# Performance work log

Hardware: AMD Instinct MI355X
Metric: run time of the kernel (lower is better)

Reference implementation:

```python
import jax, jax.numpy as jnp
import numpy as np

B, P, C = 2, 512, 21          # images, proposals/image, classes (incl background)
REG = 5                       # xc, yc, w, h, angle(deg)
DET = 100                     # detections_per_img
IMW, IMH = 1024, 800
SCORE_THRESH = 0.05
NMS_THR = 0.5
WEIGHTS = (10.0, 10.0, 5.0, 5.0, 3.0)
BBOX_XFORM_CLIP = float(np.log(1000.0 / 16.0))
MAXV = 8                      # max vertices of quad-quad intersection


def setup_inputs() -> dict:
    key = jax.random.key(0)
    k1, k2, k3 = jax.random.split(key, 3)
    class_logits = jax.random.normal(k1, (B * P, C), jnp.float32)
    box_regression = jax.random.normal(k2, (B * P, C * REG), jnp.float32)
    u = jax.random.uniform(k3, (B * P, 5), jnp.float32)
    rrects = jnp.stack([
        u[:, 0] * IMW,            # xc
        u[:, 1] * IMH,            # yc
        u[:, 2] * 200.0 + 16.0,   # w
        u[:, 3] * 200.0 + 16.0,   # h
        u[:, 4] * 360.0 - 180.0,  # angle in degrees
    ], axis=1)
    return {"class_logits": class_logits, "box_regression": box_regression, "rrects": rrects}


def rect_pts(r):
    # r [..., 5] -> corner points [..., 4, 2] (CCW quad in math coords)
    xc, yc, w, h, ang = (r[..., i] for i in range(5))
    t = ang * (jnp.pi / 180.0)
    c, s = jnp.cos(t), jnp.sin(t)
    dx, dy = w * 0.5, h * 0.5
    ox = jnp.stack([-dx, dx, dx, -dx], -1)
    oy = jnp.stack([-dy, -dy, dy, dy], -1)
    x = xc[..., None] + c[..., None] * ox - s[..., None] * oy
    y = yc[..., None] + s[..., None] * ox + c[..., None] * oy
    return jnp.stack([x, y], -1)


def decode(deltas, anchors):
    # BoxCoder.decode for rotated boxes, weights (wx,wy,ww,wh,wa)
    d = deltas.reshape(-1, C, REG) / jnp.asarray(WEIGHTS, deltas.dtype)
    dx, dy, dw, dh, da = (d[..., i] for i in range(REG))
    dw = jnp.minimum(dw, BBOX_XFORM_CLIP)
    dh = jnp.minimum(dh, BBOX_XFORM_CLIP)
    xc, yc, w, h, a = (anchors[:, i:i + 1] for i in range(5))
    px = dx * w + xc
    py = dy * h + yc
    pw = jnp.exp(dw) * w
    ph = jnp.exp(dh) * h
    pa = da * (180.0 / jnp.pi) + a
    return jnp.stack([px, py, pw, ph, pa], -1)  # [N, C, 5]


def _clip_edge(poly, n, a, b):
    # Sutherland-Hodgman clip of convex poly (buffer [MAXV,2], count n) by halfplane left of a->b
    d = b - a
    out = jnp.zeros((MAXV, 2), poly.dtype)
    m = jnp.int32(0)
    nn = jnp.maximum(n, 1)
    for i in range(MAXV):
        act = i < n
        s = poly[i]
        e = poly[jnp.mod(i + 1, nn)]
        cs = d[0] * (s[1] - a[1]) - d[1] * (s[0] - a[0])
        ce = d[0] * (e[1] - a[1]) - d[1] * (e[0] - a[0])
        denom = cs - ce
        t = cs / jnp.where(jnp.abs(denom) > 1e-12, denom, 1e-12)
        ip = s + t * (e - s)
        s_in = cs >= 0
        e_in = ce >= 0
        app1 = act & (s_in != e_in)           # crossing -> intersection point
        out = out.at[m].set(jnp.where(app1, ip, out[m]))
        m = m + app1.astype(jnp.int32)
        app2 = act & e_in                     # end point inside -> keep it
        out = out.at[m].set(jnp.where(app2, e, out[m]))
        m = m + app2.astype(jnp.int32)
    return out, m


def inter_area(p1, p2):
    # exact intersection area of two convex quads [4,2]
    poly = jnp.zeros((MAXV, 2), p1.dtype).at[:4].set(p1)
    n = jnp.int32(4)
    for k in range(4):
        poly, n = _clip_edge(poly, n, p2[k], p2[(k + 1) % 4])
    idx = jnp.arange(MAXV)
    nn = jnp.maximum(n, 1)
    nxt = jnp.mod(idx + 1, nn)
    cross = poly[:, 0] * poly[nxt, 1] - poly[nxt, 0] * poly[:, 1]
    area = 0.5 * jnp.abs(jnp.sum(jnp.where(idx < n, cross, 0.0)))
    return jnp.where(n >= 3, area, 0.0)


def _nms_one(args):
    # greedy rotated NMS on one (image,class) score-sorted set
    rr, valid = args                       # [P,5], [P] bool (sorted by desc score)
    pts = rect_pts(rr)                     # [P,4,2]
    areas = rr[:, 2] * rr[:, 3]
    inter = jax.vmap(lambda p: jax.vmap(lambda q: inter_area(p, q))(pts))(pts)
    iou = inter / (areas[:, None] + areas[None, :] - inter + 1e-8)
    n = rr.shape[0]
    def body(i, keep):
        sup = jnp.any(keep & (iou[i] > NMS_THR))
        return keep.at[i].set(valid[i] & jnp.logical_not(sup))
    return jax.lax.fori_loop(0, n, body, jnp.zeros((n,), bool))


def reference(class_logits, box_regression, rrects):
    scores = jax.nn.softmax(class_logits, -1)           # [N,C]
    proposals = decode(box_regression, rrects)          # [N,C,5]
    pts = rect_pts(proposals)                           # [N,C,4,2]
    mn, mx = pts.min(-2), pts.max(-2)
    bb = jnp.concatenate([mn, mx], -1)                  # xyxy [N,C,4]
    bb = jnp.stack([
        jnp.clip(bb[..., 0], 0.0, IMW - 1.0),
        jnp.clip(bb[..., 1], 0.0, IMH - 1.0),
        jnp.clip(bb[..., 2], 0.0, IMW - 1.0),
        jnp.clip(bb[..., 3], 0.0, IMH - 1.0),
    ], -1)

    # per-image, foreground classes only; [B, C-1, P, ...]
    sc = scores.reshape(B, P, C)[:, :, 1:].transpose(0, 2, 1)
    pr = proposals.reshape(B, P, C, 5)[:, :, 1:].transpose(0, 2, 1, 3)
    bx = bb.reshape(B, P, C, 4)[:, :, 1:].transpose(0, 2, 1, 3)

    valid = sc > SCORE_THRESH
    masked = jnp.where(valid, sc, -1.0)
    order = jnp.argsort(-masked, axis=-1)               # desc score per class
    sc_s = jnp.take_along_axis(masked, order, -1)
    valid_s = jnp.take_along_axis(valid, order, -1)
    pr_s = jnp.take_along_axis(pr, order[..., None], 2)
    bx_s = jnp.take_along_axis(bx, order[..., None], 2)

    keep = jax.lax.map(_nms_one, (jax.lax.stop_gradient(pr_s).reshape(-1, P, 5),
                                  valid_s.reshape(-1, P))).reshape(B, C - 1, P)
    keep = jax.lax.stop_gradient(keep)

    msk = jnp.where(keep, sc_s, -1.0)
    flat_s = msk.reshape(B, -1)                         # [B,(C-1)*P]
    top_idx = jax.lax.top_k(flat_s, DET)[1]
    sel_s = jnp.take_along_axis(flat_s, top_idx, -1)
    ok = sel_s > 0.0
    sel_bb = jnp.take_along_axis(bx_s.reshape(B, -1, 4), top_idx[..., None], 1)
    sel_rr = jnp.take_along_axis(pr_s.reshape(B, -1, 5), top_idx[..., None], 1)
    lab = jnp.broadcast_to(jnp.arange(1, C, dtype=jnp.int32)[:, None], (C - 1, P)).reshape(-1)
    sel_lab = lab[top_idx]

    out_bb = jnp.where(ok[..., None], sel_bb, 0.0)
    out_rr = jnp.where(ok[..., None], sel_rr, 0.0)
    out_sc = jnp.where(ok, sel_s, 0.0)
    out_lab = jnp.where(ok, sel_lab, 0)
    return out_bb, out_rr, out_sc, out_lab
```

## Files before the change

kernel.cpp:

```cpp
#include <hip/hip_runtime.h>
#include <stdint.h>

#pragma clang fp contract(off)

#define B_ 2
#define P_ 512
#define C_ 21
#define CF 20
#define DET 100
#define SCORE_THRESH 0.05f
#define NMS_THR 0.5f
#define BBOX_CLIP 4.135166556742356f
#define NC (CF * DET)

typedef unsigned long long u64;
typedef unsigned int u32;

__device__ __forceinline__ u32 f2o(float f) {
  u32 u = __float_as_uint(f);
  return (u & 0x80000000u) ? ~u : (u | 0x80000000u);
}
__device__ __forceinline__ float o2f(u32 o) {
  u32 u = (o & 0x80000000u) ? (o ^ 0x80000000u) : ~o;
  return __uint_as_float(u);
}

__global__ void __launch_bounds__(512)
prep_kernel(const float* __restrict__ logits,
            const float* __restrict__ breg,
            const float* __restrict__ rrects,
            float* __restrict__ scsS,
            float* __restrict__ ptsS,
            float* __restrict__ aabbS,
            float* __restrict__ pr5S,
            float* __restrict__ areaS,
            int* __restrict__ gV,
            u64* __restrict__ sup) {
  int g = blockIdx.x;
  int b = g / CF, cf = g % CF, c = cf + 1;
  int tid = threadIdx.x;
  int w = tid >> 6, lane = tid & 63;

  __shared__ u64 ckey[P_ + 8];
  __shared__ int wcnt[8];

  int p = tid;
  int n = b * P_ + p;
  const float* lgp = logits + n * C_;
  float lg[C_];
  #pragma unroll
  for (int k = 0; k < C_; ++k) lg[k] = lgp[k];
  float mx = lg[0];
  #pragma unroll
  for (int k = 1; k < C_; ++k) mx = fmaxf(mx, lg[k]);
  float den = 0.f, num = 0.f;
  #pragma unroll
  for (int k = 0; k < C_; ++k) {
    float ex = expf(lg[k] - mx);
    den += ex;
    num = (k == c) ? ex : num;
  }
  float sc = num / den;

  const float* d = breg + n * (C_ * 5) + c * 5;
  float dx = d[0] / 10.0f, dy = d[1] / 10.0f;
  float dw = d[2] / 5.0f, dh = d[3] / 5.0f, da = d[4] / 3.0f;
  dw = fminf(dw, BBOX_CLIP);
  dh = fminf(dh, BBOX_CLIP);
  const float* an = rrects + n * 5;
  float px = dx * an[2] + an[0];
  float py = dy * an[3] + an[1];
  float pw = expf(dw) * an[2];
  float ph = expf(dh) * an[3];
  float pa = da * 57.29577951308232f + an[4];
  float area = pw * ph;

  float t = pa * 0.017453292519943295f;
  float cs = cosf(t), sn = sinf(t);
  float hx = pw * 0.5f, hy = ph * 0.5f;
  float ox[4] = {-hx, hx, hx, -hx};
  float oy[4] = {-hy, -hy, hy, hy};
  float X[4], Y[4];
  float minx = 1e30f, miny = 1e30f, maxx = -1e30f, maxy = -1e30f;
  #pragma unroll
  for (int q = 0; q < 4; ++q) {
    float x = px + cs * ox[q] - sn * oy[q];
    float y = py + sn * ox[q] + cs * oy[q];
    X[q] = x; Y[q] = y;
    minx = fminf(minx, x); maxx = fmaxf(maxx, x);
    miny = fminf(miny, y); maxy = fmaxf(maxy, y);
  }

  bool valid = sc > SCORE_THRESH;
  float v = valid ? sc : -1.0f;
  u64 key = ((u64)f2o(v) << 32) | (u32)(~(u32)p);

  u64 m = __ballot(valid);
  if (lane == 0) wcnt[w] = __popcll(m);

  for (int z = tid; z < P_ * 8; z += 512) sup[(size_t)g * P_ * 8 + z] = 0ull;
  __syncthreads();

  int V = 0, myb = 0;
  #pragma unroll
  for (int si = 0; si < 8; ++si) {
    int cnti = wcnt[si];
    myb += (si < w) ? cnti : 0;
    V += cnti;
  }
  int slot = myb + __popcll(m & ((1ull << lane) - 1ull));
  if (valid) ckey[slot] = key;
  if (tid < 8) ckey[V + tid] = 0ull;
  __syncthreads();

  int Vr = (V + 3) & ~3;
  int r = 0;
  for (int s = 0; s < Vr; s += 4) {
    u64 a0 = ckey[s], a1 = ckey[s + 1], a2 = ckey[s + 2], a3 = ckey[s + 3];
    r += (a0 > key) ? 1 : 0;
    r += (a1 > key) ? 1 : 0;
    r += (a2 > key) ? 1 : 0;
    r += (a3 > key) ? 1 : 0;
  }

  if (valid) {
    int so = g * P_ + r;
    scsS[so] = v;
    ((float4*)ptsS)[so * 2]     = make_float4(X[0], X[1], X[2], X[3]);
    ((float4*)ptsS)[so * 2 + 1] = make_float4(Y[0], Y[1], Y[2], Y[3]);
    ((float4*)aabbS)[so] = make_float4(minx, miny, maxx, maxy);
    pr5S[so * 5 + 0] = px; pr5S[so * 5 + 1] = py;
    pr5S[so * 5 + 2] = pw; pr5S[so * 5 + 3] = ph;
    pr5S[so * 5 + 4] = pa;
    areaS[so] = area;
  }
  if (tid == 0) gV[g] = V;
}

__device__ __forceinline__ float inter_area_reg(const float qx[4], const float qy[4],
                                                const float rx[4], const float ry[4]) {
  float px_[8], py_[8];
  #pragma unroll
  for (int t = 0; t < 8; ++t) { px_[t] = (t < 4) ? qx[t] : 0.f; py_[t] = (t < 4) ? qy[t] : 0.f; }
  int n = 4;
  #pragma unroll
  for (int e = 0; e < 4; ++e) {
    float a0 = rx[e], a1 = ry[e];
    float b0 = rx[(e + 1) & 3], b1 = ry[(e + 1) & 3];
    float dx = b0 - a0, dy = b1 - a1;
    float ox_[8], oy_[8];
    #pragma unroll
    for (int t = 0; t < 8; ++t) { ox_[t] = 0.f; oy_[t] = 0.f; }
    float cr[8];
    #pragma unroll
    for (int t = 0; t < 8; ++t) cr[t] = dx * (py_[t] - a1) - dy * (px_[t] - a0);
    int m = 0;
    int nn = (n > 1) ? n : 1;
    #pragma unroll
    for (int t = 0; t < 8; ++t) {
      bool act = t < n;
      float sx = px_[t], sy = py_[t];
      float ex, ey, ce;
      if (t == 7) { ex = px_[0]; ey = py_[0]; ce = cr[0]; }
      else {
        bool wrap = (t + 1 == nn);
        ex = wrap ? px_[0] : px_[t + 1];
        ey = wrap ? py_[0] : py_[t + 1];
        ce = wrap ? cr[0] : cr[t + 1];
      }
      float cs = cr[t];
      float denom = cs - ce;
      float dn = (fabsf(denom) > 1e-12f) ? denom : 1e-12f;
      float tt = cs / dn;
      float ipx = sx + tt * (ex - sx);
      float ipy = sy + tt * (ey - sy);
      bool s_in = cs >= 0.f, e_in = ce >= 0.f;
      bool app1 = act && (s_in != e_in);
      #pragma unroll
      for (int s2 = 0; s2 < 8; ++s2) {
        bool wr = app1 && (m == s2);
        ox_[s2] = wr ? ipx : ox_[s2];
        oy_[s2] = wr ? ipy : oy_[s2];
      }
      m += app1 ? 1 : 0;
      bool app2 = act && e_in;
      #pragma unroll
      for (int s2 = 0; s2 < 8; ++s2) {
        bool wr = app2 && (m == s2);
        ox_[s2] = wr ? ex : ox_[s2];
        oy_[s2] = wr ? ey : oy_[s2];
      }
      m += app2 ? 1 : 0;
    }
    n = m;
    #pragma unroll
    for (int t = 0; t < 8; ++t) { px_[t] = ox_[t]; py_[t] = oy_[t]; }
  }
  int nn = (n > 1) ? n : 1;
  float s = 0.f;
  #pragma unroll
  for (int t = 0; t < 8; ++t) {
    if (t < n) {
      float nx_x, nx_y;
      if (t == 7) { nx_x = px_[0]; nx_y = py_[0]; }
      else {
        bool wrap = (t + 1 == nn);
        nx_x = wrap ? px_[0] : px_[t + 1];
        nx_y = wrap ? py_[0] : py_[t + 1];
      }
      s += px_[t] * nx_y - nx_x * py_[t];
    }
  }
  float area = 0.5f * fabsf(s);
  return (n >= 3) ? area : 0.f;
}

#define PPT 4
#define TPB 256
__global__ void pair_kernel(const int* __restrict__ gV,
                            const float* __restrict__ aabbS,
                            const float* __restrict__ areaS,
                            const float* __restrict__ ptsS,
                            u64* __restrict__ sup) {
  int g = blockIdx.y;
  int V = gV[g];
  int Tp = V * (V - 1) / 2;
  int base = blockIdx.x * (TPB * PPT);
  if (base >= Tp) return;
  __shared__ u32 q[TPB * PPT];
  __shared__ int qn;
  int tid = threadIdx.x;
  if (tid == 0) qn = 0;
  __syncthreads();
  const float4* ab = (const float4*)aabbS;
  for (int t = 0; t < PPT; ++t) {
    int kk = base + t * TPB + tid;
    if (kk >= Tp) break;
    float kf = (float)kk;
    int i = (int)((1.0f + sqrtf(1.0f + 8.0f * kf)) * 0.5f);
    while (i * (i - 1) / 2 > kk) --i;
    while ((i + 1) * i / 2 <= kk) ++i;
    int j = kk - i * (i - 1) / 2;
    float4 bi = ab[g * P_ + i];
    float4 bj = ab[g * P_ + j];
    bool ov = (bi.x <= bj.z) && (bj.x <= bi.z) && (bi.y <= bj.w) && (bj.y <= bi.w);
    if (ov) {
      int s = atomicAdd(&qn, 1);
      q[s] = (u32)((i << 9) | j);
    }
  }
  __syncthreads();
  int nq = qn;
  const float4* pS = (const float4*)ptsS;
  for (int s = tid; s < nq; s += TPB) {
    u32 pk = q[s];
    int i = (int)(pk >> 9), j = (int)(pk & 511);
    float4 ax = pS[(g * P_ + i) * 2];
    float4 ay = pS[(g * P_ + i) * 2 + 1];
    float4 bx = pS[(g * P_ + j) * 2];
    float4 by = pS[(g * P_ + j) * 2 + 1];
    float qx[4] = {ax.x, ax.y, ax.z, ax.w};
    float qy[4] = {ay.x, ay.y, ay.z, ay.w};
    float rx[4] = {bx.x, bx.y, bx.z, bx.w};
    float ry[4] = {by.x, by.y, by.z, by.w};
    float ai = areaS[g * P_ + i];
    float aj = areaS[g * P_ + j];
    float inter = inter_area_reg(qx, qy, rx, ry);
    float iou = inter / (((ai + aj) - inter) + 1e-8f);
    if (iou > NMS_THR)
      atomicOr(&sup[((size_t)g * P_ + i) * 8 + (j >> 6)], 1ull << (j & 63));
  }
}

__global__ void greedy_kernel(const float* __restrict__ scsS, const int* __restrict__ gV,
                              const float* __restrict__ aabbS, const float* __restrict__ pr5S,
                              const u64* __restrict__ sup,
                              u64* __restrict__ cand, float* __restrict__ rec) {
  int g = blockIdx.x;
  int tid = threadIdx.x;
  __shared__ u64 lsup[P_ * 8];
  __shared__ u32 skeep[16];
  int V = gV[g];
  for (int w = tid; w < V * 8; w += 64) lsup[w] = sup[(size_t)g * P_ * 8 + w];
  __syncthreads();
  u64 keepw = 0;
  u64 cur = (tid < 8 && V > 0) ? lsup[tid] : 0ull;
  for (int i = 0; i < V; ++i) {
    u64 nxt = (tid < 8 && (i + 1) < V) ? lsup[(i + 1) * 8 + tid] : 0ull;
    bool supd = __any((cur & keepw) != 0ull);
    if (!supd && tid == (i >> 6)) keepw |= 1ull << (i & 63);
    cur = nxt;
  }
  if (tid < 8) { skeep[tid * 2] = (u32)keepw; skeep[tid * 2 + 1] = (u32)(keepw >> 32); }
  __syncthreads();
  int cls = g % CF;
  int tot = 0;
  #pragma unroll
  for (int t = 0; t < 16; ++t) tot += __popc(skeep[t]);
  for (int r = tid; r < V; r += 64) {
    if ((skeep[r >> 5] >> (r & 31)) & 1u) {
      int slot = __popc(skeep[r >> 5] & ((1u << (r & 31)) - 1u));
      for (int t = 0; t < (r >> 5); ++t) slot += __popc(skeep[t]);
      if (slot < DET) {
        float sv = scsS[g * P_ + r];
        int flat = cls * P_ + r;
        cand[g * DET + slot] = ((u64)f2o(sv) << 32) | (u32)(~(u32)flat);
        int so = g * P_ + r;
        float* rr = rec + (size_t)(g * DET + slot) * 12;
        rr[0] = fminf(fmaxf(aabbS[so * 4 + 0], 0.f), 1023.0f);
        rr[1] = fminf(fmaxf(aabbS[so * 4 + 1], 0.f), 799.0f);
        rr[2] = fminf(fmaxf(aabbS[so * 4 + 2], 0.f), 1023.0f);
        rr[3] = fminf(fmaxf(aabbS[so * 4 + 3], 0.f), 799.0f);
        rr[4] = pr5S[so * 5 + 0]; rr[5] = pr5S[so * 5 + 1]; rr[6] = pr5S[so * 5 + 2];
        rr[7] = pr5S[so * 5 + 3]; rr[8] = pr5S[so * 5 + 4];
        rr[9] = sv;
        rr[10] = (float)(cls + 1);
        rr[11] = 0.f;
      }
    }
  }
  int fill = tot < DET ? tot : DET;
  for (int s = fill + tid; s < DET; s += 64) cand[g * DET + s] = 0ull;
}

__global__ void rank_kernel(const u64* __restrict__ cand, const float* __restrict__ rec,
                            float* __restrict__ out) {
  int b = blockIdx.y;
  int tid = threadIdx.x;
  __shared__ u64 lc[NC];
  __shared__ int ncand;
  if (tid == 0) ncand = 0;
  __syncthreads();
  int nz = 0;
  for (int i = tid; i < NC; i += 256) {
    u64 v = cand[b * NC + i];
    lc[i] = v;
    nz += (v != 0ull) ? 1 : 0;
  }
  u64 m = __ballot(nz > 0);
  if (nz > 0) atomicAdd(&ncand, nz);
  (void)m;
  __syncthreads();
  int ci = blockIdx.x * 256 + tid;
  if (ci >= NC) return;
  if (blockIdx.x == 0 && tid < DET && tid >= ncand) {
    int o_bb = (b * DET + tid) * 4;
    int o_rr = B_ * DET * 4 + (b * DET + tid) * 5;
    int o_sc = B_ * DET * 9 + b * DET + tid;
    int o_lab = B_ * DET * 10 + b * DET + tid;
    out[o_bb + 0] = 0.f; out[o_bb + 1] = 0.f; out[o_bb + 2] = 0.f; out[o_bb + 3] = 0.f;
    out[o_rr + 0] = 0.f; out[o_rr + 1] = 0.f; out[o_rr + 2] = 0.f;
    out[o_rr + 3] = 0.f; out[o_rr + 4] = 0.f;
    out[o_sc] = 0.f;
    out[o_lab] = 0.f;
  }
  u64 k = lc[ci];
  if (k == 0ull) return;
  int rank = 0;
  #pragma unroll
  for (int gp = 0; gp < CF; ++gp) {
    int lo = 0, hi = DET;
    while (lo < hi) {
      int mid = (lo + hi) >> 1;
      if (lc[gp * DET + mid] > k) lo = mid + 1; else hi = mid;
    }
    rank += lo;
  }
  if (rank >= DET) return;
  const float* rr = rec + (size_t)(b * NC + ci) * 12;
  int o_bb = (b * DET + rank) * 4;
  int o_rr = B_ * DET * 4 + (b * DET + rank) * 5;
  int o_sc = B_ * DET * 9 + b * DET + rank;
  int o_lab = B_ * DET * 10 + b * DET + rank;
  out[o_bb + 0] = rr[0]; out[o_bb + 1] = rr[1];
  out[o_bb + 2] = rr[2]; out[o_bb + 3] = rr[3];
  out[o_rr + 0] = rr[4]; out[o_rr + 1] = rr[5]; out[o_rr + 2] = rr[6];
  out[o_rr + 3] = rr[7]; out[o_rr + 4] = rr[8];
  out[o_sc] = rr[9];
  out[o_lab] = rr[10];
}

extern "C" void kernel_launch(void* const* d_in, const int* in_sizes, int n_in,
                              void* d_out, int out_size, void* d_ws, size_t ws_size,
                              hipStream_t stream) {
  const float* logits = (const float*)d_in[0];
  const float* breg   = (const float*)d_in[1];
  const float* rrects = (const float*)d_in[2];
  float* out = (float*)d_out;

  const int G = B_ * CF;
  u64*   sup  = (u64*)d_ws;
  u64*   cand = sup + (size_t)G * P_ * 8;
  int*   gV   = (int*)(cand + G * DET);
  float* scsS = (float*)(gV + 64);
  float* ptsS = scsS + (size_t)G * P_;
  float* aabbS = ptsS + (size_t)G * P_ * 8;
  float* pr5S = aabbS + (size_t)G * P_ * 4;
  float* areaS = pr5S + (size_t)G * P_ * 5;
  float* rec  = areaS + (size_t)G * P_;

  prep_kernel<<<G, 512, 0, stream>>>(logits, breg, rrects,
                                     scsS, ptsS, aabbS, pr5S, areaS, gV, sup);
  pair_kernel<<<dim3(128, G), TPB, 0, stream>>>(gV, aabbS, areaS, ptsS, sup);
  greedy_kernel<<<G, 64, 0, stream>>>(scsS, gV, aabbS, pr5S, sup, cand, rec);
  rank_kernel<<<dim3((NC + 255) / 256, B_), 256, 0, stream>>>(cand, rec, out);
}
```

Measured before the change: 129.0 us.

## Fuse prep, pairwise IoU and greedy NMS into one per-class kernel

```diff
diff --git a/kernel.cpp b/kernel.cpp
--- a/kernel.cpp
+++ b/kernel.cpp
@@ -12,6 +12,7 @@
 #define NMS_THR 0.5f
 #define BBOX_CLIP 4.135166556742356f
 #define NC (CF * DET)
+#define CH 4096
 
 typedef unsigned long long u64;
 typedef unsigned int u32;
@@ -19,122 +20,6 @@
 __device__ __forceinline__ u32 f2o(float f) {
   u32 u = __float_as_uint(f);
   return (u & 0x80000000u) ? ~u : (u | 0x80000000u);
-}
-__device__ __forceinline__ float o2f(u32 o) {
-  u32 u = (o & 0x80000000u) ? (o ^ 0x80000000u) : ~o;
-  return __uint_as_float(u);
-}
-
-__global__ void __launch_bounds__(512)
-prep_kernel(const float* __restrict__ logits,
-            const float* __restrict__ breg,
-            const float* __restrict__ rrects,
-            float* __restrict__ scsS,
-            float* __restrict__ ptsS,
-            float* __restrict__ aabbS,
-            float* __restrict__ pr5S,
-            float* __restrict__ areaS,
-            int* __restrict__ gV,
-            u64* __restrict__ sup) {
-  int g = blockIdx.x;
-  int b = g / CF, cf = g % CF, c = cf + 1;
-  int tid = threadIdx.x;
-  int w = tid >> 6, lane = tid & 63;
-
-  __shared__ u64 ckey[P_ + 8];
-  __shared__ int wcnt[8];
-
-  int p = tid;
-  int n = b * P_ + p;
-  const float* lgp = logits + n * C_;
-  float lg[C_];
-  #pragma unroll
-  for (int k = 0; k < C_; ++k) lg[k] = lgp[k];
-  float mx = lg[0];
-  #pragma unroll
-  for (int k = 1; k < C_; ++k) mx = fmaxf(mx, lg[k]);
-  float den = 0.f, num = 0.f;
-  #pragma unroll
-  for (int k = 0; k < C_; ++k) {
-    float ex = expf(lg[k] - mx);
-    den += ex;
-    num = (k == c) ? ex : num;
-  }
-  float sc = num / den;
-
-  const float* d = breg + n * (C_ * 5) + c * 5;
-  float dx = d[0] / 10.0f, dy = d[1] / 10.0f;
-  float dw = d[2] / 5.0f, dh = d[3] / 5.0f, da = d[4] / 3.0f;
-  dw = fminf(dw, BBOX_CLIP);
-  dh = fminf(dh, BBOX_CLIP);
-  const float* an = rrects + n * 5;
-  float px = dx * an[2] + an[0];
-  float py = dy * an[3] + an[1];
-  float pw = expf(dw) * an[2];
-  float ph = expf(dh) * an[3];
-  float pa = da * 57.29577951308232f + an[4];
-  float area = pw * ph;
-
-  float t = pa * 0.017453292519943295f;
-  float cs = cosf(t), sn = sinf(t);
-  float hx = pw * 0.5f, hy = ph * 0.5f;
-  float ox[4] = {-hx, hx, hx, -hx};
-  float oy[4] = {-hy, -hy, hy, hy};
-  float X[4], Y[4];
-  float minx = 1e30f, miny = 1e30f, maxx = -1e30f, maxy = -1e30f;
-  #pragma unroll
-  for (int q = 0; q < 4; ++q) {
-    float x = px + cs * ox[q] - sn * oy[q];
-    float y = py + sn * ox[q] + cs * oy[q];
-    X[q] = x; Y[q] = y;
-    minx = fminf(minx, x); maxx = fmaxf(maxx, x);
-    miny = fminf(miny, y); maxy = fmaxf(maxy, y);
-  }
-
-  bool valid = sc > SCORE_THRESH;
-  float v = valid ? sc : -1.0f;
-  u64 key = ((u64)f2o(v) << 32) | (u32)(~(u32)p);
-
-  u64 m = __ballot(valid);
-  if (lane == 0) wcnt[w] = __popcll(m);
-
-  for (int z = tid; z < P_ * 8; z += 512) sup[(size_t)g * P_ * 8 + z] = 0ull;
-  __syncthreads();
-
-  int V = 0, myb = 0;
-  #pragma unroll
-  for (int si = 0; si < 8; ++si) {
-    int cnti = wcnt[si];
-    myb += (si < w) ? cnti : 0;
-    V += cnti;
-  }
-  int slot = myb + __popcll(m & ((1ull << lane) - 1ull));
-  if (valid) ckey[slot] = key;
-  if (tid < 8) ckey[V + tid] = 0ull;
-  __syncthreads();
-
-  int Vr = (V + 3) & ~3;
-  int r = 0;
-  for (int s = 0; s < Vr; s += 4) {
-    u64 a0 = ckey[s], a1 = ckey[s + 1], a2 = ckey[s + 2], a3 = ckey[s + 3];
-    r += (a0 > key) ? 1 : 0;
-    r += (a1 > key) ? 1 : 0;
-    r += (a2 > key) ? 1 : 0;
-    r += (a3 > key) ? 1 : 0;
-  }
-
-  if (valid) {
-    int so = g * P_ + r;
-    scsS[so] = v;
-    ((float4*)ptsS)[so * 2]     = make_float4(X[0], X[1], X[2], X[3]);
-    ((float4*)ptsS)[so * 2 + 1] = make_float4(Y[0], Y[1], Y[2], Y[3]);
-    ((float4*)aabbS)[so] = make_float4(minx, miny, maxx, maxy);
-    pr5S[so * 5 + 0] = px; pr5S[so * 5 + 1] = py;
-    pr5S[so * 5 + 2] = pw; pr5S[so * 5 + 3] = ph;
-    pr5S[so * 5 + 4] = pa;
-    areaS[so] = area;
-  }
-  if (tid == 0) gV[g] = V;
 }
 
 __device__ __forceinline__ float inter_area_reg(const float qx[4], const float qy[4],
@@ -215,112 +100,204 @@
   return (n >= 3) ? area : 0.f;
 }
 
-#define PPT 4
-#define TPB 256
-__global__ void pair_kernel(const int* __restrict__ gV,
-                            const float* __restrict__ aabbS,
-                            const float* __restrict__ areaS,
-                            const float* __restrict__ ptsS,
-                            u64* __restrict__ sup) {
-  int g = blockIdx.y;
-  int V = gV[g];
+__global__ void __launch_bounds__(512)
+fused_kernel(const float* __restrict__ logits,
+             const float* __restrict__ breg,
+             const float* __restrict__ rrects,
+             u64* __restrict__ cand, float* __restrict__ rec) {
+  int g = blockIdx.x;
+  int b = g / CF, cf = g % CF, c = cf + 1;
+  int tid = threadIdx.x;
+  int w = tid >> 6, lane = tid & 63;
+
+  __shared__ u64 ckey[P_ + 8];
+  __shared__ int wcnt[8];
+  __shared__ float scs[P_];
+  __shared__ float4 ptsX[P_];
+  __shared__ float4 ptsY[P_];
+  __shared__ float4 aabb[P_];
+  __shared__ float pr5[P_ * 5];
+  __shared__ float areaL[P_];
+  __shared__ u32 lsup[P_ * 16];
+  __shared__ u32 q[CH];
+  __shared__ int qn;
+  __shared__ u32 skeep[16];
+
+  int p = tid;
+  int n = b * P_ + p;
+  const float* lgp = logits + n * C_;
+  float lg[C_];
+  #pragma unroll
+  for (int k = 0; k < C_; ++k) lg[k] = lgp[k];
+  float mx = lg[0];
+  #pragma unroll
+  for (int k = 1; k < C_; ++k) mx = fmaxf(mx, lg[k]);
+  float den = 0.f, num = 0.f;
+  #pragma unroll
+  for (int k = 0; k < C_; ++k) {
+    float ex = expf(lg[k] - mx);
+    den += ex;
+    num = (k == c) ? ex : num;
+  }
+  float sc = num / den;
+
+  const float* d = breg + n * (C_ * 5) + c * 5;
+  float dx = d[0] / 10.0f, dy = d[1] / 10.0f;
+  float dw = d[2] / 5.0f, dh = d[3] / 5.0f, da = d[4] / 3.0f;
+  dw = fminf(dw, BBOX_CLIP);
+  dh = fminf(dh, BBOX_CLIP);
+  const float* an = rrects + n * 5;
+  float px = dx * an[2] + an[0];
+  float py = dy * an[3] + an[1];
+  float pw = expf(dw) * an[2];
+  float ph = expf(dh) * an[3];
+  float pa = da * 57.29577951308232f + an[4];
+  float area = pw * ph;
+
+  float t = pa * 0.017453292519943295f;
+  float cs = cosf(t), sn = sinf(t);
+  float hx = pw * 0.5f, hy = ph * 0.5f;
+  float ox[4] = {-hx, hx, hx, -hx};
+  float oy[4] = {-hy, -hy, hy, hy};
+  float X[4], Y[4];
+  float minx = 1e30f, miny = 1e30f, maxx = -1e30f, maxy = -1e30f;
+  #pragma unroll
+  for (int qq = 0; qq < 4; ++qq) {
+    float x = px + cs * ox[qq] - sn * oy[qq];
+    float y = py + sn * ox[qq] + cs * oy[qq];
+    X[qq] = x; Y[qq] = y;
+    minx = fminf(minx, x); maxx = fmaxf(maxx, x);
+    miny = fminf(miny, y); maxy = fmaxf(maxy, y);
+  }
+
+  bool valid = sc > SCORE_THRESH;
+  float v = valid ? sc : -1.0f;
+  u64 key = ((u64)f2o(v) << 32) | (u32)(~(u32)p);
+
+  u64 m = __ballot(valid);
+  if (lane == 0) wcnt[w] = __popcll(m);
+
+  for (int z = tid; z < P_ * 16; z += 512) lsup[z] = 0u;
+  __syncthreads();
+
+  int V = 0, myb = 0;
+  #pragma unroll
+  for (int si = 0; si < 8; ++si) {
+    int cnti = wcnt[si];
+    myb += (si < w) ? cnti : 0;
+    V += cnti;
+  }
+  int slot = myb + __popcll(m & ((1ull << lane) - 1ull));
+  if (valid) ckey[slot] = key;
+  if (tid < 8) ckey[V + tid] = 0ull;
+  __syncthreads();
+
+  int Vr = (V + 3) & ~3;
+  int r = 0;
+  for (int s = 0; s < Vr; s += 4) {
+    u64 a0 = ckey[s], a1 = ckey[s + 1], a2 = ckey[s + 2], a3 = ckey[s + 3];
+    r += (a0 > key) ? 1 : 0;
+    r += (a1 > key) ? 1 : 0;
+    r += (a2 > key) ? 1 : 0;
+    r += (a3 > key) ? 1 : 0;
+  }
+  if (valid) {
+    scs[r] = v;
+    ptsX[r] = make_float4(X[0], X[1], X[2], X[3]);
+    ptsY[r] = make_float4(Y[0], Y[1], Y[2], Y[3]);
+    aabb[r] = make_float4(minx, miny, maxx, maxy);
+    pr5[r * 5 + 0] = px; pr5[r * 5 + 1] = py;
+    pr5[r * 5 + 2] = pw; pr5[r * 5 + 3] = ph;
+    pr5[r * 5 + 4] = pa;
+    areaL[r] = area;
+  }
+  __syncthreads();
+
   int Tp = V * (V - 1) / 2;
-  int base = blockIdx.x * (TPB * PPT);
-  if (base >= Tp) return;
-  __shared__ u32 q[TPB * PPT];
-  __shared__ int qn;
-  int tid = threadIdx.x;
-  if (tid == 0) qn = 0;
-  __syncthreads();
-  const float4* ab = (const float4*)aabbS;
-  for (int t = 0; t < PPT; ++t) {
-    int kk = base + t * TPB + tid;
-    if (kk >= Tp) break;
-    float kf = (float)kk;
-    int i = (int)((1.0f + sqrtf(1.0f + 8.0f * kf)) * 0.5f);
-    while (i * (i - 1) / 2 > kk) --i;
-    while ((i + 1) * i / 2 <= kk) ++i;
-    int j = kk - i * (i - 1) / 2;
-    float4 bi = ab[g * P_ + i];
-    float4 bj = ab[g * P_ + j];
-    bool ov = (bi.x <= bj.z) && (bj.x <= bi.z) && (bi.y <= bj.w) && (bj.y <= bi.w);
-    if (ov) {
-      int s = atomicAdd(&qn, 1);
-      q[s] = (u32)((i << 9) | j);
-    }
-  }
-  __syncthreads();
-  int nq = qn;
-  const float4* pS = (const float4*)ptsS;
-  for (int s = tid; s < nq; s += TPB) {
-    u32 pk = q[s];
-    int i = (int)(pk >> 9), j = (int)(pk & 511);
-    float4 ax = pS[(g * P_ + i) * 2];
-    float4 ay = pS[(g * P_ + i) * 2 + 1];
-    float4 bx = pS[(g * P_ + j) * 2];
-    float4 by = pS[(g * P_ + j) * 2 + 1];
-    float qx[4] = {ax.x, ax.y, ax.z, ax.w};
-    float qy[4] = {ay.x, ay.y, ay.z, ay.w};
-    float rx[4] = {bx.x, bx.y, bx.z, bx.w};
-    float ry[4] = {by.x, by.y, by.z, by.w};
-    float ai = areaS[g * P_ + i];
-    float aj = areaS[g * P_ + j];
-    float inter = inter_area_reg(qx, qy, rx, ry);
-    float iou = inter / (((ai + aj) - inter) + 1e-8f);
-    if (iou > NMS_THR)
-      atomicOr(&sup[((size_t)g * P_ + i) * 8 + (j >> 6)], 1ull << (j & 63));
-  }
-}
-
-__global__ void greedy_kernel(const float* __restrict__ scsS, const int* __restrict__ gV,
-                              const float* __restrict__ aabbS, const float* __restrict__ pr5S,
-                              const u64* __restrict__ sup,
-                              u64* __restrict__ cand, float* __restrict__ rec) {
-  int g = blockIdx.x;
-  int tid = threadIdx.x;
-  __shared__ u64 lsup[P_ * 8];
-  __shared__ u32 skeep[16];
-  int V = gV[g];
-  for (int w = tid; w < V * 8; w += 64) lsup[w] = sup[(size_t)g * P_ * 8 + w];
-  __syncthreads();
-  u64 keepw = 0;
-  u64 cur = (tid < 8 && V > 0) ? lsup[tid] : 0ull;
-  for (int i = 0; i < V; ++i) {
-    u64 nxt = (tid < 8 && (i + 1) < V) ? lsup[(i + 1) * 8 + tid] : 0ull;
-    bool supd = __any((cur & keepw) != 0ull);
-    if (!supd && tid == (i >> 6)) keepw |= 1ull << (i & 63);
-    cur = nxt;
-  }
-  if (tid < 8) { skeep[tid * 2] = (u32)keepw; skeep[tid * 2 + 1] = (u32)(keepw >> 32); }
-  __syncthreads();
-  int cls = g % CF;
+  for (int base = 0; base < Tp; base += CH) {
+    if (tid == 0) qn = 0;
+    __syncthreads();
+    #pragma unroll
+    for (int tchunk = 0; tchunk < CH / 512; ++tchunk) {
+      int kk = base + tchunk * 512 + tid;
+      if (kk < Tp) {
+        float kf = (float)kk;
+        int i = (int)((1.0f + sqrtf(1.0f + 8.0f * kf)) * 0.5f);
+        while (i * (i - 1) / 2 > kk) --i;
+        while ((i + 1) * i / 2 <= kk) ++i;
+        int j = kk - i * (i - 1) / 2;
+        float4 bi = aabb[i];
+        float4 bj = aabb[j];
+        bool ov = (bi.x <= bj.z) && (bj.x <= bi.z) && (bi.y <= bj.w) && (bj.y <= bi.w);
+        if (ov) {
+          int s = atomicAdd(&qn, 1);
+          q[s] = (u32)((i << 9) | j);
+        }
+      }
+    }
+    __syncthreads();
+    int nq = qn;
+    for (int s = tid; s < nq; s += 512) {
+      u32 pk = q[s];
+      int i = (int)(pk >> 9), j = (int)(pk & 511);
+      float4 ax = ptsX[i], ay = ptsY[i];
+      float4 bx = ptsX[j], by = ptsY[j];
+      float qx[4] = {ax.x, ax.y, ax.z, ax.w};
+      float qy[4] = {ay.x, ay.y, ay.z, ay.w};
+      float rx[4] = {bx.x, bx.y, bx.z, bx.w};
+      float ry[4] = {by.x, by.y, by.z, by.w};
+      float ai = areaL[i];
+      float aj = areaL[j];
+      float inter = inter_area_reg(qx, qy, rx, ry);
+      float iou = inter / (((ai + aj) - inter) + 1e-8f);
+      if (iou > NMS_THR)
+        atomicOr(&lsup[i * 16 + (j >> 5)], 1u << (j & 31));
+    }
+    __syncthreads();
+  }
+
+  if (tid < 64) {
+    u32 keepw = 0;
+    u32 cur = (tid < 16 && V > 0) ? lsup[tid] : 0u;
+    for (int i = 0; i < V; ++i) {
+      u32 nxt = (tid < 16 && (i + 1) < V) ? lsup[(i + 1) * 16 + tid] : 0u;
+      bool supd = __any((cur & keepw) != 0u);
+      if (!supd && tid == (i >> 5)) keepw |= 1u << (i & 31);
+      cur = nxt;
+    }
+    if (tid < 16) skeep[tid] = keepw;
+  }
+  __syncthreads();
+
   int tot = 0;
   #pragma unroll
-  for (int t = 0; t < 16; ++t) tot += __popc(skeep[t]);
-  for (int r = tid; r < V; r += 64) {
-    if ((skeep[r >> 5] >> (r & 31)) & 1u) {
-      int slot = __popc(skeep[r >> 5] & ((1u << (r & 31)) - 1u));
-      for (int t = 0; t < (r >> 5); ++t) slot += __popc(skeep[t]);
-      if (slot < DET) {
-        float sv = scsS[g * P_ + r];
-        int flat = cls * P_ + r;
-        cand[g * DET + slot] = ((u64)f2o(sv) << 32) | (u32)(~(u32)flat);
-        int so = g * P_ + r;
-        float* rr = rec + (size_t)(g * DET + slot) * 12;
-        rr[0] = fminf(fmaxf(aabbS[so * 4 + 0], 0.f), 1023.0f);
-        rr[1] = fminf(fmaxf(aabbS[so * 4 + 1], 0.f), 799.0f);
-        rr[2] = fminf(fmaxf(aabbS[so * 4 + 2], 0.f), 1023.0f);
-        rr[3] = fminf(fmaxf(aabbS[so * 4 + 3], 0.f), 799.0f);
-        rr[4] = pr5S[so * 5 + 0]; rr[5] = pr5S[so * 5 + 1]; rr[6] = pr5S[so * 5 + 2];
-        rr[7] = pr5S[so * 5 + 3]; rr[8] = pr5S[so * 5 + 4];
-        rr[9] = sv;
-        rr[10] = (float)(cls + 1);
-        rr[11] = 0.f;
+  for (int t2 = 0; t2 < 16; ++t2) tot += __popc(skeep[t2]);
+  int rr_i = tid;
+  if (rr_i < V) {
+    if ((skeep[rr_i >> 5] >> (rr_i & 31)) & 1u) {
+      int oslot = __popc(skeep[rr_i >> 5] & ((1u << (rr_i & 31)) - 1u));
+      for (int t2 = 0; t2 < (rr_i >> 5); ++t2) oslot += __popc(skeep[t2]);
+      if (oslot < DET) {
+        float sv = scs[rr_i];
+        int flat = cf * P_ + rr_i;
+        cand[g * DET + oslot] = ((u64)f2o(sv) << 32) | (u32)(~(u32)flat);
+        float* rrp = rec + (size_t)(g * DET + oslot) * 12;
+        float4 ab4 = aabb[rr_i];
+        rrp[0] = fminf(fmaxf(ab4.x, 0.f), 1023.0f);
+        rrp[1] = fminf(fmaxf(ab4.y, 0.f), 799.0f);
+        rrp[2] = fminf(fmaxf(ab4.z, 0.f), 1023.0f);
+        rrp[3] = fminf(fmaxf(ab4.w, 0.f), 799.0f);
+        rrp[4] = pr5[rr_i * 5 + 0]; rrp[5] = pr5[rr_i * 5 + 1];
+        rrp[6] = pr5[rr_i * 5 + 2]; rrp[7] = pr5[rr_i * 5 + 3];
+        rrp[8] = pr5[rr_i * 5 + 4];
+        rrp[9] = sv;
+        rrp[10] = (float)(cf + 1);
+        rrp[11] = 0.f;
       }
     }
   }
   int fill = tot < DET ? tot : DET;
-  for (int s = fill + tid; s < DET; s += 64) cand[g * DET + s] = 0ull;
+  for (int s = fill + tid; s < DET; s += 512) cand[g * DET + s] = 0ull;
 }
 
 __global__ void rank_kernel(const u64* __restrict__ cand, const float* __restrict__ rec,
@@ -337,9 +314,7 @@
     lc[i] = v;
     nz += (v != 0ull) ? 1 : 0;
   }
-  u64 m = __ballot(nz > 0);
   if (nz > 0) atomicAdd(&ncand, nz);
-  (void)m;
   __syncthreads();
   int ci = blockIdx.x * 256 + tid;
   if (ci >= NC) return;
@@ -389,19 +364,9 @@
   float* out = (float*)d_out;
 
   const int G = B_ * CF;
-  u64*   sup  = (u64*)d_ws;
-  u64*   cand = sup + (size_t)G * P_ * 8;
-  int*   gV   = (int*)(cand + G * DET);
-  float* scsS = (float*)(gV + 64);
-  float* ptsS = scsS + (size_t)G * P_;
-  float* aabbS = ptsS + (size_t)G * P_ * 8;
-  float* pr5S = aabbS + (size_t)G * P_ * 4;
-  float* areaS = pr5S + (size_t)G * P_ * 5;
-  float* rec  = areaS + (size_t)G * P_;
-
-  prep_kernel<<<G, 512, 0, stream>>>(logits, breg, rrects,
-                                     scsS, ptsS, aabbS, pr5S, areaS, gV, sup);
-  pair_kernel<<<dim3(128, G), TPB, 0, stream>>>(gV, aabbS, areaS, ptsS, sup);
-  greedy_kernel<<<G, 64, 0, stream>>>(scsS, gV, aabbS, pr5S, sup, cand, rec);
+  u64*   cand = (u64*)d_ws;
+  float* rec  = (float*)(cand + G * DET);
+
+  fused_kernel<<<G, 512, 0, stream>>>(logits, breg, rrects, cand, rec);
   rank_kernel<<<dim3((NC + 255) / 256, B_), 256, 0, stream>>>(cand, rec, out);
 }
```

Result: slower. 147.8 us (+14.5%).
